# Performance work log

Measured on AMD Instinct MI355X. Metric: run time of the kernel, lower is better.

The kernel has to match this reference:

```python
import jax, jax.numpy as jnp
import numpy as np

IN_FEATURES = 4096
OUT_FEATURES = 11008
GROUP_SIZE = 128
NUM_GROUPS = IN_FEATURES // GROUP_SIZE  # 32


def setup_inputs() -> dict:
    key = jax.random.key(0)
    k1, k2, k3, k4, k5 = jax.random.split(key, 5)
    x = jax.random.normal(k1, (4, 2048, IN_FEATURES), dtype=jnp.float32)
    # packed 4-bit weights: each int holds (high << 4) | low, values in [0, 256)
    qweight = jax.random.randint(k2, (IN_FEATURES // 2, OUT_FEATURES), 0, 256, dtype=jnp.int32)
    scales = jax.random.uniform(k3, (NUM_GROUPS, OUT_FEATURES), dtype=jnp.float32) * 0.01 + 1e-4
    zeros = jax.random.normal(k4, (NUM_GROUPS, OUT_FEATURES), dtype=jnp.float32) * 0.01
    bias = jax.random.normal(k5, (OUT_FEATURES,), dtype=jnp.float32) * 0.01
    return {"x": x, "qweight": qweight, "scales": scales, "zeros": zeros, "bias": bias}


def _dequantize(qweight, scales, zeros, dtype):
    # unpack two 4-bit values per byte; even input rows = low nibble, odd = high nibble
    low = ((qweight & 15) - 8).astype(dtype)          # [in/2, out]
    high = (((qweight >> 4) & 15) - 8).astype(dtype)  # [in/2, out]
    w = jnp.stack([low, high], axis=1).reshape(IN_FEATURES, OUT_FEATURES)
    # per-group affine dequant: w = q * scale + zero
    w = w.reshape(NUM_GROUPS, GROUP_SIZE, OUT_FEATURES)
    w = w * scales[:, None, :] + zeros[:, None, :]
    return w.reshape(IN_FEATURES, OUT_FEATURES)


def reference(x, qweight, scales, zeros, bias):
    weight = _dequantize(qweight, scales, zeros, x.dtype)  # [in, out]
    # F.linear(x, weight.T, bias) == x @ weight + bias
    return jnp.einsum('bsi,io->bso', x, weight) + bias
```

## Files before the change

### kernel.cpp

```cpp
#include <hip/hip_runtime.h>
#include <hip/hip_bf16.h>

#define IN_F 4096
#define OUT_F 11008
#define GSIZE 128
#define M_TOTAL 8192

typedef float f32x4 __attribute__((ext_vector_type(4)));
typedef float f32x16 __attribute__((ext_vector_type(16)));
typedef unsigned short u16x8 __attribute__((ext_vector_type(8)));
typedef unsigned int u32x4 __attribute__((ext_vector_type(4)));
typedef __bf16 bf16x8 __attribute__((ext_vector_type(8)));

#define ASG __attribute__((address_space(1)))
#define ASL __attribute__((address_space(3)))

__device__ __forceinline__ unsigned short f2bf(float f) {
    union { float f; unsigned int u; } v;
    v.f = f;
    unsigned int u = v.u;
    unsigned int r = (u + 0x7fffu + ((u >> 16) & 1u)) >> 16;
    return (unsigned short)r;
}


__global__ void convert_x_frag_kernel(const float* __restrict__ x,
                                      unsigned short* __restrict__ xb) {
    const int mf = blockIdx.x;
    const int r  = threadIdx.x >> 3;
    const int kb = (threadIdx.x & 7) * 8;
    const int k0 = blockIdx.y * 512;
    const float* src = x + (size_t)(mf * 32 + r) * IN_F;
    unsigned short* dst = xb + (size_t)mf * (IN_F / 16) * 512;
#pragma unroll
    for (int kk = 0; kk < 512; kk += 64) {
        const int k = k0 + kk + kb;
        f32x4 a = *(const f32x4*)(src + k);
        f32x4 b = *(const f32x4*)(src + k + 4);
        u16x8 v;
#pragma unroll
        for (int e = 0; e < 4; ++e) {
            v[e]     = f2bf(a[e]);
            v[e + 4] = f2bf(b[e]);
        }
        const int kf = k >> 4, q2 = (k >> 3) & 1;
        *(u16x8*)(dst + (size_t)kf * 512 + (q2 * 32 + r) * 8) = v;
    }
}

__global__ void dequant_w_frag_kernel(const int* __restrict__ qw,
                                      const float* __restrict__ scales,
                                      const float* __restrict__ zeros,
                                      unsigned short* __restrict__ wt) {
    const int n  = blockIdx.x * 256 + threadIdx.x;
    const int k0 = blockIdx.y * 32;
    const int g  = k0 >> 7;
    const float s = scales[(size_t)g * OUT_F + n];
    const float z = zeros[(size_t)g * OUT_F + n];

    unsigned short outv[32];
#pragma unroll
    for (int i = 0; i < 16; ++i) {
        int q = qw[(size_t)(k0 / 2 + i) * OUT_F + n];
        float lo = (float)((q & 15) - 8) * s + z;
        float hi = (float)(((q >> 4) & 15) - 8) * s + z;
        outv[2 * i]     = f2bf(lo);
        outv[2 * i + 1] = f2bf(hi);
    }
    const int nf = n >> 5, r32 = n & 31;
    unsigned short* base = wt + (size_t)nf * (IN_F / 16) * 512 +
                           (size_t)(k0 >> 4) * 512;
    const u16x8* sv = (const u16x8*)outv;
#pragma unroll
    for (int c = 0; c < 4; ++c)
        *(u16x8*)(base + (c >> 1) * 512 + ((c & 1) * 32 + r32) * 8) = sv[c];
}

__global__ void dequant_w_rowmajor_kernel(const int* __restrict__ qw,
                                          const float* __restrict__ scales,
                                          const float* __restrict__ zeros,
                                          unsigned short* __restrict__ wt) {
    const int n  = blockIdx.x * 256 + threadIdx.x;
    const int k0 = blockIdx.y * 32;
    const int g  = k0 >> 7;
    const float s = scales[(size_t)g * OUT_F + n];
    const float z = zeros[(size_t)g * OUT_F + n];

    unsigned short outv[32];
#pragma unroll
    for (int i = 0; i < 16; ++i) {
        int q = qw[(size_t)(k0 / 2 + i) * OUT_F + n];
        float lo = (float)((q & 15) - 8) * s + z;
        float hi = (float)(((q >> 4) & 15) - 8) * s + z;
        outv[2 * i]     = f2bf(lo);
        outv[2 * i + 1] = f2bf(hi);
    }
    u16x8* dst = (u16x8*)(wt + (size_t)n * IN_F + k0);
    const u16x8* src = (const u16x8*)outv;
#pragma unroll
    for (int i = 0; i < 4; ++i) dst[i] = src[i];
}

__global__ __launch_bounds__(512, 1)
void gemm_8phase(const unsigned short* __restrict__ xb,
                 const unsigned short* __restrict__ wt,
                 const float* __restrict__ bias,
                 float* __restrict__ out) {
    constexpr int NT = IN_F / 64;
    constexpr int NKF = IN_F / 16;
    __shared__ __attribute__((aligned(128))) unsigned short lds[65536];

    constexpr int NB_N = OUT_F / 256;
    constexpr int NWG  = (M_TOTAL / 256) * NB_N;
    constexpr int CPX  = NWG / 8;
    const int wg = ((int)blockIdx.x % 8) * CPX + (int)blockIdx.x / 8;
    const int m0 = (wg / NB_N) * 256;
    const int n0 = (wg % NB_N) * 256;

    const int tid  = threadIdx.x;
    const int lane = tid & 63;
    const int wave = tid >> 6;
    const int wr = wave >> 2;
    const int wc = wave & 3;
    const int r32 = lane & 31;
    const int q2  = lane >> 5;

    const ASG char* xbc = (const ASG char*)xb;
    const ASG char* wtc = (const ASG char*)wt;
    ASL char* ldsc = (ASL char*)lds;

    const int mfb = m0 >> 5;
    const int nfb = n0 >> 5;
    unsigned int oA[4], oB[4];
    int dA[4], dB[4];
#pragma unroll
    for (int H = 0; H < 2; ++H)
#pragma unroll
        for (int i = 0; i < 2; ++i) {
            const int s = i * 8 + wave;
            const int rf = s >> 2, kc = s & 3;
            oA[H * 2 + i] = (unsigned int)(((mfb + H * 4 + rf) * NKF + kc) * 1024 +
                                           lane * 16);
            dA[H * 2 + i] = (H * 16 + s) * 1024;
        }
#pragma unroll
    for (int G = 0; G < 2; ++G)
#pragma unroll
        for (int i = 0; i < 2; ++i) {
            const int s = i * 8 + wave;
            const int cf = (s >> 2) * 2 + G, kc = s & 3;
            oB[G * 2 + i] = (unsigned int)(((nfb + cf) * NKF + kc) * 1024 +
                                           lane * 16);
            dB[G * 2 + i] = 32768 + (cf * 4 + kc) * 1024;
        }

#define STG_A(H, P)                                                            \
    do {                                                                       \
        _Pragma("unroll") for (int _i = 0; _i < 2; ++_i)                       \
            __builtin_amdgcn_global_load_lds(                                  \
                (ASG const unsigned int*)(xbc + oA[(H) * 2 + _i]),             \
                (ASL unsigned int*)(ldsc + dA[(H) * 2 + _i] + (P) * 65536),    \
                16, 0, 0);                                                     \
    } while (0)
#define STG_BG(G, P)                                                           \
    do {                                                                       \
        _Pragma("unroll") for (int _i = 0; _i < 2; ++_i)                       \
            __builtin_amdgcn_global_load_lds(                                  \
                (ASG const unsigned int*)(wtc + oB[(G) * 2 + _i]),             \
                (ASL unsigned int*)(ldsc + dB[(G) * 2 + _i] + (P) * 65536),    \
                16, 0, 0);                                                     \
    } while (0)
#define ADV_A(H) do { oA[(H)*2] += 4096; oA[(H)*2+1] += 4096; } while (0)
#define ADV_BG(G) do { oB[(G)*2] += 4096; oB[(G)*2+1] += 4096; } while (0)

#define BAR()                                                                  \
    do {                                                                       \
        __builtin_amdgcn_sched_barrier(0);                                     \
        __builtin_amdgcn_s_barrier();                                          \
        __builtin_amdgcn_sched_barrier(0);                                     \
    } while (0)

    bf16x8 afH0[2][4], afH1[2][4];
    bf16x8 bfE[4], bfO[4];
    f32x16 acc[4][2];
#pragma unroll
    for (int i = 0; i < 4; ++i)
#pragma unroll
        for (int j = 0; j < 2; ++j) acc[i][j] = (f32x16)0.0f;

#define READ_A0(P)                                                             \
    do {                                                                       \
        const unsigned short* _ab = lds + (P) * 32768 + lane * 8;              \
        _Pragma("unroll") for (int _m = 0; _m < 2; ++_m)                       \
        _Pragma("unroll") for (int _kc = 0; _kc < 4; ++_kc)                    \
            afH0[_m][_kc] = *(const bf16x8*)(_ab +                             \
                (((wr * 4 + _m) * 4 + _kc) << 9));                             \
    } while (0)
#define READ_A1(P)                                                             \
    do {                                                                       \
        const unsigned short* _ab = lds + (P) * 32768 + lane * 8;              \
        _Pragma("unroll") for (int _m = 0; _m < 2; ++_m)                       \
        _Pragma("unroll") for (int _kc = 0; _kc < 4; ++_kc)                    \
            afH1[_m][_kc] = *(const bf16x8*)(_ab +                             \
                (((wr * 4 + 2 + _m) * 4 + _kc) << 9));                         \
    } while (0)
#define READ_BLO(P)                                                            \
    do {                                                                       \
        const unsigned short* _bb = lds + (P) * 32768 + 16384 + lane * 8;      \
        _Pragma("unroll") for (int _kc = 0; _kc < 4; ++_kc)                    \
            bfE[_kc] = *(const bf16x8*)(_bb +                                  \
                (((wc * 2) * 4 + _kc) << 9));                                  \
    } while (0)
#define READ_BHI(P)                                                            \
    do {                                                                       \
        const unsigned short* _bb = lds + (P) * 32768 + 16384 + lane * 8;      \
        _Pragma("unroll") for (int _kc = 0; _kc < 4; ++_kc)                    \
            bfO[_kc] = *(const bf16x8*)(_bb +                                  \
                (((wc * 2 + 1) * 4 + _kc) << 9));                              \
    } while (0)

#define QUADX(AF, BF, MH, NH)                                                  \
    do {                                                                       \
        __builtin_amdgcn_s_setprio(1);                                         \
        _Pragma("unroll") for (int _m = 0; _m < 2; ++_m)                       \
        _Pragma("unroll") for (int _kc = 0; _kc < 4; ++_kc)                    \
            acc[(MH) * 2 + _m][(NH)] =                                         \
                __builtin_amdgcn_mfma_f32_32x32x16_bf16(                       \
                    AF[_m][_kc], BF[_kc], acc[(MH) * 2 + _m][(NH)], 0, 0, 0);  \
        __builtin_amdgcn_s_setprio(0);                                         \
    } while (0)

    STG_BG(0, 0); ADV_BG(0);
    STG_BG(1, 0); ADV_BG(1);
    STG_A(0, 0);  ADV_A(0);
    STG_A(1, 0);  ADV_A(1);
    STG_BG(0, 1); ADV_BG(0);
    STG_BG(1, 1); ADV_BG(1);
    STG_A(0, 1);  ADV_A(0);
    __builtin_amdgcn_sched_barrier(0);
    asm volatile("s_waitcnt vmcnt(6)" ::: "memory");
    BAR();

#pragma unroll 1
    for (int tt = 0; tt < NT; tt += 2) {
        const bool g2 = (tt + 2 < NT);
        const bool g3 = (tt + 3 < NT);
        READ_A0(0);
        READ_BLO(0);
        STG_A(1, 1); ADV_A(1);
        BAR();
        QUADX(afH0, bfE, 0, 0);
        READ_BHI(0);
        if (g2) STG_BG(0, 0);
        ADV_BG(0);
        BAR();
        QUADX(afH0, bfO, 0, 1);
        READ_A1(0);
        if (g2) STG_BG(1, 0);
        ADV_BG(1);
        BAR();
        QUADX(afH1, bfE, 1, 0);
        if (g2) STG_A(0, 0);
        ADV_A(0);
        __builtin_amdgcn_sched_barrier(0);
        if (tt < NT - 2) {
            asm volatile("s_waitcnt vmcnt(6)" ::: "memory");
        } else {
            asm volatile("s_waitcnt vmcnt(0)" ::: "memory");
        }
        BAR();
        QUADX(afH1, bfO, 1, 1);
        READ_A0(1);
        READ_BLO(1);
        if (g2) STG_A(1, 0);
        ADV_A(1);
        BAR();
        QUADX(afH0, bfE, 0, 0);
        READ_BHI(1);
        if (g3) STG_BG(0, 1);
        ADV_BG(0);
        BAR();
        QUADX(afH0, bfO, 0, 1);
        READ_A1(1);
        if (g3) STG_BG(1, 1);
        ADV_BG(1);
        BAR();
        QUADX(afH1, bfE, 1, 0);
        if (g3) STG_A(0, 1);
        ADV_A(0);
        __builtin_amdgcn_sched_barrier(0);
        if (tt + 1 < NT - 2) {
            asm volatile("s_waitcnt vmcnt(6)" ::: "memory");
        } else {
            asm volatile("s_waitcnt vmcnt(0)" ::: "memory");
        }
        BAR();
        QUADX(afH1, bfO, 1, 1);
    }

#pragma unroll
    for (int nf = 0; nf < 2; ++nf) {
        const int col = n0 + wc * 64 + nf * 32 + r32;
        const float bv = bias[col];
#pragma unroll
        for (int mf = 0; mf < 4; ++mf) {
            const int row0 = m0 + wr * 128 + mf * 32 + q2 * 4;
#pragma unroll
            for (int r = 0; r < 16; ++r) {
                const int row = row0 + (r & 3) + ((r >> 2) << 3);
                __builtin_nontemporal_store(acc[mf][nf][r] + bv,
                                            &out[(size_t)row * OUT_F + col]);
            }
        }
    }
#undef STG_A
#undef STG_BG
#undef ADV_A
#undef ADV_BG
#undef BAR
#undef READ_A0
#undef READ_A1
#undef READ_BLO
#undef READ_BHI
#undef QUADX
}

template <bool PREW>
__global__ __launch_bounds__(256, 2)
void gemm_kernel(const float* __restrict__ x,
                 const unsigned short* __restrict__ wt,
                 const int* __restrict__ qw,
                 const float* __restrict__ scales,
                 const float* __restrict__ zeros,
                 const float* __restrict__ bias,
                 float* __restrict__ out) {
    constexpr int BM = 128, BN = 128, BK = 64;
    constexpr int LDK = BK + 8;
    constexpr int NT = IN_F / BK;

    __shared__ unsigned short As[BM * LDK];
    __shared__ unsigned short Bs[BN * LDK];

    const int bid = blockIdx.x;
    constexpr int NB_N = OUT_F / BN;
    const int m0 = (bid / NB_N) * BM;
    const int n0 = (bid % NB_N) * BN;

    const int tid  = threadIdx.x;
    const int lane = tid & 63;
    const int wave = tid >> 6;
    const int wr = wave >> 1, wc = wave & 1;

    const int st_row = tid >> 3;
    const int st_col = (tid & 7) * 8;

    f32x4 areg[4][2];
    u32x4 breg[4];
    int   qreg[16];
    float s_, z_;
    const int b_n  = tid & 127;
    const int b_kp = (tid >> 7) * 16;

    auto load_tile = [&](int kt) {
        {
            const float* base = x + (size_t)m0 * IN_F + (size_t)kt * BK + st_col;
#pragma unroll
            for (int p = 0; p < 4; ++p) {
                const float* rp = base + (size_t)(p * 32 + st_row) * IN_F;
                areg[p][0] = *(const f32x4*)rp;
                areg[p][1] = *(const f32x4*)(rp + 4);
            }
        }
        if constexpr (PREW) {
            const unsigned short* base = wt + (size_t)n0 * IN_F + (size_t)kt * BK + st_col;
#pragma unroll
            for (int p = 0; p < 4; ++p)
                breg[p] = *(const u32x4*)(base + (size_t)(p * 32 + st_row) * IN_F);
        } else {
            const int kp0 = kt * (BK / 2) + b_kp;
#pragma unroll
            for (int i = 0; i < 16; ++i)
                qreg[i] = qw[(size_t)(kp0 + i) * OUT_F + n0 + b_n];
            const int g = (kt * BK) >> 7;
            s_ = scales[(size_t)g * OUT_F + n0 + b_n];
            z_ = zeros[(size_t)g * OUT_F + n0 + b_n];
        }
    };

    auto write_lds = [&]() {
#pragma unroll
        for (int p = 0; p < 4; ++p) {
            u16x8 v;
#pragma unroll
            for (int e = 0; e < 4; ++e) {
                v[e]     = f2bf(areg[p][0][e]);
                v[e + 4] = f2bf(areg[p][1][e]);
            }
            *(u16x8*)(&As[(p * 32 + st_row) * LDK + st_col]) = v;
        }
        if constexpr (PREW) {
#pragma unroll
            for (int p = 0; p < 4; ++p)
                *(u32x4*)(&Bs[(p * 32 + st_row) * LDK + st_col]) = breg[p];
        } else {
            unsigned short tmp[32];
#pragma unroll
            for (int i = 0; i < 16; ++i) {
                int q = qreg[i];
                tmp[2 * i]     = f2bf((float)((q & 15) - 8) * s_ + z_);
                tmp[2 * i + 1] = f2bf((float)(((q >> 4) & 15) - 8) * s_ + z_);
            }
            const u16x8* srcv = (const u16x8*)tmp;
#pragma unroll
            for (int i = 0; i < 4; ++i)
                *(u16x8*)(&Bs[b_n * LDK + 2 * b_kp + 8 * i]) = srcv[i];
        }
    };

    f32x4 acc[4][4];
#pragma unroll
    for (int i = 0; i < 4; ++i)
#pragma unroll
        for (int j = 0; j < 4; ++j) acc[i][j] = (f32x4)0.0f;

    load_tile(0);

#pragma unroll 1
    for (int kt = 0; kt < NT; ++kt) {
        __syncthreads();
        write_lds();
        __syncthreads();
        if (kt + 1 < NT) load_tile(kt + 1);

#pragma unroll
        for (int kk = 0; kk < 2; ++kk) {
            const int kidx = kk * 32 + ((lane >> 4) << 3);
            bf16x8 afv[4], bfv[4];
#pragma unroll
            for (int i = 0; i < 4; ++i)
                afv[i] = *(const bf16x8*)(&As[(wr * 64 + i * 16 + (lane & 15)) * LDK + kidx]);
#pragma unroll
            for (int j = 0; j < 4; ++j)
                bfv[j] = *(const bf16x8*)(&Bs[(wc * 64 + j * 16 + (lane & 15)) * LDK + kidx]);
#pragma unroll
            for (int i = 0; i < 4; ++i)
#pragma unroll
                for (int j = 0; j < 4; ++j)
                    acc[i][j] = __builtin_amdgcn_mfma_f32_16x16x32_bf16(afv[i], bfv[j], acc[i][j], 0, 0, 0);
        }
    }

    const int orow_base = m0 + wr * 64 + ((lane >> 4) << 2);
    const int ocol_base = n0 + wc * 64 + (lane & 15);
#pragma unroll
    for (int j = 0; j < 4; ++j) {
        const float bv = bias[ocol_base + j * 16];
#pragma unroll
        for (int i = 0; i < 4; ++i) {
#pragma unroll
            for (int q = 0; q < 4; ++q) {
                out[(size_t)(orow_base + i * 16 + q) * OUT_F + (ocol_base + j * 16)] =
                    acc[i][j][q] + bv;
            }
        }
    }
}

extern "C" void kernel_launch(void* const* d_in, const int* in_sizes, int n_in,
                              void* d_out, int out_size, void* d_ws, size_t ws_size,
                              hipStream_t stream) {
    const float* x      = (const float*)d_in[0];
    const int*   qw     = (const int*)d_in[1];
    const float* scales = (const float*)d_in[2];
    const float* zeros  = (const float*)d_in[3];
    const float* bias   = (const float*)d_in[4];
    float* out = (float*)d_out;

    const size_t wt_bytes = (size_t)OUT_F * IN_F * sizeof(unsigned short);
    const size_t xb_bytes = (size_t)M_TOTAL * IN_F * sizeof(unsigned short);

    if (ws_size >= wt_bytes + xb_bytes) {
        unsigned short* wt = (unsigned short*)d_ws;
        unsigned short* xb = (unsigned short*)((char*)d_ws + wt_bytes);
        convert_x_frag_kernel<<<dim3(M_TOTAL / 32, 8), 256, 0, stream>>>(x, xb);
        dequant_w_frag_kernel<<<dim3(OUT_F / 256, IN_F / 32), 256, 0, stream>>>(qw, scales, zeros, wt);
        gemm_8phase<<<(M_TOTAL / 256) * (OUT_F / 256), 512, 0, stream>>>(xb, wt, bias, out);
    } else if (ws_size >= wt_bytes) {
        unsigned short* wt = (unsigned short*)d_ws;
        dequant_w_rowmajor_kernel<<<dim3(OUT_F / 256, IN_F / 32), 256, 0, stream>>>(qw, scales, zeros, wt);
        gemm_kernel<true><<<(M_TOTAL / 128) * (OUT_F / 128), 256, 0, stream>>>(x, wt, qw, scales, zeros, bias, out);
    } else {
        gemm_kernel<false><<<(M_TOTAL / 128) * (OUT_F / 128), 256, 0, stream>>>(x, nullptr, qw, scales, zeros, bias, out);
    }
}
```

Baseline: 719.5 us.

## Rebalance LDS fragment reads evenly across the eight GEMM phases

Result: slower. 824.4 us (+14.6%).

```diff
diff --git a/kernel.cpp b/kernel.cpp
--- a/kernel.cpp
+++ b/kernel.cpp
@@ -102,10 +102,10 @@
 }
 
 __global__ __launch_bounds__(512, 1)
-void gemm_8phase(const unsigned short* __restrict__ xb,
-                 const unsigned short* __restrict__ wt,
-                 const float* __restrict__ bias,
-                 float* __restrict__ out) {
+void gemm_bal(const unsigned short* __restrict__ xb,
+              const unsigned short* __restrict__ wt,
+              const float* __restrict__ bias,
+              float* __restrict__ out) {
     constexpr int NT = IN_F / 64;
     constexpr int NKF = IN_F / 16;
     __shared__ __attribute__((aligned(128))) unsigned short lds[65536];
@@ -188,36 +188,12 @@
 #pragma unroll
         for (int j = 0; j < 2; ++j) acc[i][j] = (f32x16)0.0f;
 
-#define READ_A0(P)                                                             \
-    do {                                                                       \
-        const unsigned short* _ab = lds + (P) * 32768 + lane * 8;              \
-        _Pragma("unroll") for (int _m = 0; _m < 2; ++_m)                       \
-        _Pragma("unroll") for (int _kc = 0; _kc < 4; ++_kc)                    \
-            afH0[_m][_kc] = *(const bf16x8*)(_ab +                             \
-                (((wr * 4 + _m) * 4 + _kc) << 9));                             \
-    } while (0)
-#define READ_A1(P)                                                             \
-    do {                                                                       \
-        const unsigned short* _ab = lds + (P) * 32768 + lane * 8;              \
-        _Pragma("unroll") for (int _m = 0; _m < 2; ++_m)                       \
-        _Pragma("unroll") for (int _kc = 0; _kc < 4; ++_kc)                    \
-            afH1[_m][_kc] = *(const bf16x8*)(_ab +                             \
-                (((wr * 4 + 2 + _m) * 4 + _kc) << 9));                         \
-    } while (0)
-#define READ_BLO(P)                                                            \
-    do {                                                                       \
-        const unsigned short* _bb = lds + (P) * 32768 + 16384 + lane * 8;      \
-        _Pragma("unroll") for (int _kc = 0; _kc < 4; ++_kc)                    \
-            bfE[_kc] = *(const bf16x8*)(_bb +                                  \
-                (((wc * 2) * 4 + _kc) << 9));                                  \
-    } while (0)
-#define READ_BHI(P)                                                            \
-    do {                                                                       \
-        const unsigned short* _bb = lds + (P) * 32768 + 16384 + lane * 8;      \
-        _Pragma("unroll") for (int _kc = 0; _kc < 4; ++_kc)                    \
-            bfO[_kc] = *(const bf16x8*)(_bb +                                  \
-                (((wc * 2 + 1) * 4 + _kc) << 9));                              \
-    } while (0)
+#define RDA(P, M_, KC, DST)                                                    \
+    DST = *(const bf16x8*)(lds + (P) * 32768 + lane * 8 +                      \
+                           (((wr * 4 + (M_)) * 4 + (KC)) << 9))
+#define RDB(P, NF, KC, DST)                                                    \
+    DST = *(const bf16x8*)(lds + (P) * 32768 + 16384 + lane * 8 +              \
+                           (((wc * 2 + (NF)) * 4 + (KC)) << 9))
 
 #define QUADX(AF, BF, MH, NH)                                                  \
     do {                                                                       \
@@ -230,73 +206,92 @@
         __builtin_amdgcn_s_setprio(0);                                         \
     } while (0)
 
+#define RD_PRE(P)                         \
+    do { RDA(P,0,0,afH0[0][0]); RDA(P,0,1,afH0[0][1]);                         \
+         RDA(P,0,2,afH0[0][2]); RDA(P,0,3,afH0[0][3]);                         \
+         RDA(P,1,0,afH0[1][0]); RDA(P,1,1,afH0[1][1]); } while (0)
+#define RD_Z0(P)                              \
+    do { RDA(P,1,2,afH0[1][2]); RDA(P,1,3,afH0[1][3]);                         \
+         RDB(P,0,0,bfE[0]); RDB(P,0,1,bfE[1]);                                 \
+         RDB(P,0,2,bfE[2]); RDB(P,0,3,bfE[3]); } while (0)
+#define RD_Z1(P)                              \
+    do { RDB(P,1,0,bfO[0]); RDB(P,1,1,bfO[1]);                                 \
+         RDB(P,1,2,bfO[2]); RDB(P,1,3,bfO[3]);                                 \
+         RDA(P,2,0,afH1[0][0]); RDA(P,2,1,afH1[0][1]); } while (0)
+#define RD_Z2(P)                          \
+    do { RDA(P,2,2,afH1[0][2]); RDA(P,2,3,afH1[0][3]);                         \
+         RDA(P,3,0,afH1[1][0]); RDA(P,3,1,afH1[1][1]);                         \
+         RDA(P,3,2,afH1[1][2]); RDA(P,3,3,afH1[1][3]); } while (0)
+
     STG_BG(0, 0); ADV_BG(0);
     STG_BG(1, 0); ADV_BG(1);
+    STG_A(1, 0);  ADV_A(1);
     STG_A(0, 0);  ADV_A(0);
-    STG_A(1, 0);  ADV_A(1);
     STG_BG(0, 1); ADV_BG(0);
     STG_BG(1, 1); ADV_BG(1);
-    STG_A(0, 1);  ADV_A(0);
+    STG_A(1, 1);  ADV_A(1);
     __builtin_amdgcn_sched_barrier(0);
     asm volatile("s_waitcnt vmcnt(6)" ::: "memory");
     BAR();
+    RD_PRE(0);
 
 #pragma unroll 1
     for (int tt = 0; tt < NT; tt += 2) {
         const bool g2 = (tt + 2 < NT);
         const bool g3 = (tt + 3 < NT);
-        READ_A0(0);
-        READ_BLO(0);
-        STG_A(1, 1); ADV_A(1);
+        if (tt > 0) QUADX(afH1, bfO, 1, 1);
+        RD_Z0(0);
+        STG_A(0, 1); ADV_A(0);
         BAR();
         QUADX(afH0, bfE, 0, 0);
-        READ_BHI(0);
+        RD_Z1(0);
         if (g2) STG_BG(0, 0);
         ADV_BG(0);
         BAR();
         QUADX(afH0, bfO, 0, 1);
-        READ_A1(0);
+        RD_Z2(0);
         if (g2) STG_BG(1, 0);
         ADV_BG(1);
+        __builtin_amdgcn_sched_barrier(0);
+        if (g2) {
+            asm volatile("s_waitcnt vmcnt(4)" ::: "memory");
+        } else {
+            asm volatile("s_waitcnt vmcnt(0)" ::: "memory");
+        }
         BAR();
         QUADX(afH1, bfE, 1, 0);
+        RD_PRE(1);
+        if (g2) STG_A(1, 0);
+        ADV_A(1);
+        BAR();
+        QUADX(afH1, bfO, 1, 1);
+        RD_Z0(1);
         if (g2) STG_A(0, 0);
         ADV_A(0);
+        BAR();
+        QUADX(afH0, bfE, 0, 0);
+        RD_Z1(1);
+        if (g3) STG_BG(0, 1);
+        ADV_BG(0);
+        BAR();
+        QUADX(afH0, bfO, 0, 1);
+        RD_Z2(1);
+        if (g3) STG_BG(1, 1);
+        ADV_BG(1);
         __builtin_amdgcn_sched_barrier(0);
-        if (tt < NT - 2) {
-            asm volatile("s_waitcnt vmcnt(6)" ::: "memory");
+        if (g3) {
+            asm volatile("s_waitcnt vmcnt(4)" ::: "memory");
         } else {
             asm volatile("s_waitcnt vmcnt(0)" ::: "memory");
         }
         BAR();
-        QUADX(afH1, bfO, 1, 1);
-        READ_A0(1);
-        READ_BLO(1);
-        if (g2) STG_A(1, 0);
+        QUADX(afH1, bfE, 1, 0);
+        if (g2) RD_PRE(0);
+        if (g3) STG_A(1, 1);
         ADV_A(1);
         BAR();
-        QUADX(afH0, bfE, 0, 0);
-        READ_BHI(1);
-        if (g3) STG_BG(0, 1);
-        ADV_BG(0);
-        BAR();
-        QUADX(afH0, bfO, 0, 1);
-        READ_A1(1);
-        if (g3) STG_BG(1, 1);
-        ADV_BG(1);
-        BAR();
-        QUADX(afH1, bfE, 1, 0);
-        if (g3) STG_A(0, 1);
-        ADV_A(0);
-        __builtin_amdgcn_sched_barrier(0);
-        if (tt + 1 < NT - 2) {
-            asm volatile("s_waitcnt vmcnt(6)" ::: "memory");
-        } else {
-            asm volatile("s_waitcnt vmcnt(0)" ::: "memory");
-        }
-        BAR();
-        QUADX(afH1, bfO, 1, 1);
-    }
+    }
+    QUADX(afH1, bfO, 1, 1);
 
 #pragma unroll
     for (int nf = 0; nf < 2; ++nf) {
@@ -318,10 +313,12 @@
 #undef ADV_A
 #undef ADV_BG
 #undef BAR
-#undef READ_A0
-#undef READ_A1
-#undef READ_BLO
-#undef READ_BHI
+#undef RDA
+#undef RDB
+#undef RD_PRE
+#undef RD_Z0
+#undef RD_Z1
+#undef RD_Z2
 #undef QUADX
 }
 
@@ -484,7 +481,7 @@
         unsigned short* xb = (unsigned short*)((char*)d_ws + wt_bytes);
         convert_x_frag_kernel<<<dim3(M_TOTAL / 32, 8), 256, 0, stream>>>(x, xb);
         dequant_w_frag_kernel<<<dim3(OUT_F / 256, IN_F / 32), 256, 0, stream>>>(qw, scales, zeros, wt);
-        gemm_8phase<<<(M_TOTAL / 256) * (OUT_F / 256), 512, 0, stream>>>(xb, wt, bias, out);
+        gemm_bal<<<(M_TOTAL / 256) * (OUT_F / 256), 512, 0, stream>>>(xb, wt, bias, out);
     } else if (ws_size >= wt_bytes) {
         unsigned short* wt = (unsigned short*)d_ws;
         dequant_w_rowmajor_kernel<<<dim3(OUT_F / 256, IN_F / 32), 256, 0, stream>>>(qw, scales, zeros, wt);
```
